# Kernel tuning notes

Measured on AMD Instinct MI355X. Metric: run time of the kernel, lower is better.

Reference implementation:

```python
import jax, jax.numpy as jnp
import numpy as np

B, T, D, H = 4, 2048, 1024, 16
HD = D // H  # head_dim = 64

def setup_inputs() -> dict:
    key = jax.random.key(0)
    k1, k2, k3 = jax.random.split(key, 3)
    x = jax.random.normal(k1, (B, T, D), dtype=jnp.float32)
    Wqkv = jax.random.normal(k2, (D, 3 * D), dtype=jnp.float32) * (D ** -0.5)
    Wout = jax.random.normal(k3, (D, D), dtype=jnp.float32) * (D ** -0.5)
    return {"x": x, "Wqkv": Wqkv, "Wout": Wout}

def reference(x, Wqkv, Wout):
    Bb, Tt, C = x.shape
    qkv = x @ Wqkv  # [B,T,3D]
    qkv = qkv.reshape(Bb, Tt, 3, H, HD)
    q, k, v = qkv[:, :, 0], qkv[:, :, 1], qkv[:, :, 2]  # each [B,T,H,HD]
    scale = 1.0 / np.sqrt(HD)
    # scores [B,H,T,T]
    attn = jnp.einsum('bqhd,bkhd->bhqk', q, k) * scale
    causal = jnp.tril(jnp.ones((Tt, Tt), dtype=bool))
    attn = jnp.where(causal[None, None], attn, -jnp.inf)
    attn = jax.nn.softmax(attn, axis=-1)
    out = jnp.einsum('bhqk,bkhd->bqhd', attn, v).reshape(Bb, Tt, C)
    return out @ Wout
```

## Files before the change

### kernel.cpp

```cpp
#include <hip/hip_runtime.h>
#include <hip/hip_bf16.h>

#define T_SEQ 2048
#define NBATCH 4
#define NHEAD 16
#define HDIM 64
#define DMODEL 1024

typedef __bf16 bf16x8 __attribute__((ext_vector_type(8)));
typedef float f32x4 __attribute__((ext_vector_type(4)));
typedef float f32x16 __attribute__((ext_vector_type(16)));

__device__ __forceinline__ unsigned short f2bf(float f) {
  unsigned int u = __builtin_bit_cast(unsigned int, f);
  u += 0x7fffu + ((u >> 16) & 1u);
  return (unsigned short)(u >> 16);
}

__device__ __forceinline__ float fexp2(float x) {
  float r;
  asm("v_exp_f32 %0, %1" : "=v"(r) : "v"(x));
  return r;
}

__device__ __forceinline__ void async_cp16(void* lds, const void* g) {
  __builtin_amdgcn_global_load_lds((const __attribute__((address_space(1))) void*)g,
                                   (__attribute__((address_space(3))) void*)lds,
                                   16, 0, 0);
}

__global__ __launch_bounds__(256) void conv_bf16_k(const float* __restrict__ in,
                                                   unsigned short* __restrict__ out, int n) {
  int i = (blockIdx.x * 256 + threadIdx.x) * 4;
  if (i >= n) return;
  float4 v = *(const float4*)(in + i);
  ushort4 o;
  o.x = f2bf(v.x); o.y = f2bf(v.y); o.z = f2bf(v.z); o.w = f2bf(v.w);
  *(ushort4*)(out + i) = o;
}

__global__ __launch_bounds__(256) void transpose_bf16_k(const float* __restrict__ in,
                                                        unsigned short* __restrict__ out,
                                                        int R, int C) {
  __shared__ float tile[32][33];
  int c0 = blockIdx.x * 32, r0 = blockIdx.y * 32;
  int tx = threadIdx.x, ty = threadIdx.y;
#pragma unroll
  for (int j = 0; j < 32; j += 8)
    tile[ty + j][tx] = in[(size_t)(r0 + ty + j) * C + c0 + tx];
  __syncthreads();
#pragma unroll
  for (int j = 0; j < 32; j += 8)
    out[(size_t)(c0 + ty + j) * R + r0 + tx] = f2bf(tile[tx][ty + j]);
}

template <int EPI, int NT>
__global__ __launch_bounds__(512, 1) void gemm_8ph2_k(const unsigned short* __restrict__ A,
                                                      const unsigned short* __restrict__ Bt,
                                                      unsigned short* __restrict__ Qb,
                                                      unsigned short* __restrict__ Kb,
                                                      unsigned short* __restrict__ Vt,
                                                      float* __restrict__ Cout) {
  __shared__ uint4 ldsv[6144];
  char* lds = (char*)ldsv;
  const int t = threadIdx.x;
  const int w = t >> 6, lane = t & 63;
  const int lr = lane & 15, lg = lane >> 4;
  const int wr = w >> 1, wc = w & 1;
  const int bid = blockIdx.x;
  const int perx = (NT * 32) / 8;
  const int wid = (bid & 7) * perx + (bid >> 3);
  const int m0 = (wid / NT) * 256, n0 = (wid % NT) * 128;

  const int row0 = t >> 3;
  const int colc0 = (t & 7) ^ (row0 & 7);
  const int stU = w * 1024;

  const unsigned short* Abase = A + (size_t)(m0 + row0) * 1024 + colc0 * 8;
  const unsigned short* Bbase = Bt + (size_t)(n0 + row0) * 1024 + colc0 * 8;

#define STGA(dst, h, kt)                                                        \
  {                                                                             \
    const unsigned short* _s = Abase + (size_t)(h) * 128 * 1024 + (kt) * 64;    \
    async_cp16(lds + (dst) + (h) * 16384 + stU, _s);                            \
    async_cp16(lds + (dst) + (h) * 16384 + stU + 8192, _s + 64 * 1024);         \
  }
#define STGB(dst, kt)                                                           \
  {                                                                             \
    const unsigned short* _s = Bbase + (kt) * 64;                               \
    async_cp16(lds + (dst) + 32768 + stU, _s);                                  \
    async_cp16(lds + (dst) + 32768 + stU + 8192, _s + 64 * 1024);               \
  }
#define VM2() asm volatile("s_waitcnt vmcnt(2)" ::: "memory")
#define BAR()                                                                   \
  {                                                                             \
    __builtin_amdgcn_s_barrier();                                               \
    __builtin_amdgcn_sched_barrier(0);                                          \
  }

  f32x4 acc[4][4];
#pragma unroll
  for (int mi = 0; mi < 4; ++mi)
#pragma unroll
    for (int ni = 0; ni < 4; ++ni) acc[mi][ni] = (f32x4){0.f, 0.f, 0.f, 0.f};

  STGA(0, 0, 0);
  STGA(0, 1, 0);
  STGB(0, 0);
  STGB(49152, 1);
  VM2();
  BAR();

  bf16x8 bfr[4][2], af[2][2];
  const int ldsAh = (wr >> 1) * 16384;
  const int arow0 = (wr & 1) * 64;
  const int brow0 = wc * 64;

#define LDB(pbase)                                                                   \
  {                                                                                  \
    _Pragma("unroll") for (int ni = 0; ni < 4; ++ni) _Pragma("unroll")               \
        for (int kk = 0; kk < 2; ++kk) {                                             \
      int rrow = brow0 + ni * 16 + lr;                                               \
      int cc = (kk * 4 + lg) ^ (lr & 7);                                             \
      bfr[ni][kk] = *(const bf16x8*)(lds + (pbase) + 32768 + rrow * 128 + cc * 16);  \
    }                                                                                \
  }
#define LDA(Q, pbase)                                                                \
  {                                                                                  \
    _Pragma("unroll") for (int m2 = 0; m2 < 2; ++m2) _Pragma("unroll")               \
        for (int kk = 0; kk < 2; ++kk) {                                             \
      int rrow = arow0 + (2 * (Q) + m2) * 16 + lr;                                   \
      int cc = (kk * 4 + lg) ^ (lr & 7);                                             \
      af[m2][kk] = *(const bf16x8*)(lds + (pbase) + ldsAh + rrow * 128 + cc * 16);   \
    }                                                                                \
  }
#define MM(Q)                                                                        \
  {                                                                                  \
    __builtin_amdgcn_s_setprio(1);                                                   \
    _Pragma("unroll") for (int m2 = 0; m2 < 2; ++m2) _Pragma("unroll")               \
        for (int kk = 0; kk < 2; ++kk) _Pragma("unroll") for (int ni = 0; ni < 4;    \
                                                              ++ni) acc[2 * (Q) +    \
                                                                        m2][ni] =    \
            __builtin_amdgcn_mfma_f32_16x16x32_bf16(af[m2][kk], bfr[ni][kk],         \
                                                    acc[2 * (Q) + m2][ni], 0, 0, 0); \
    __builtin_amdgcn_s_setprio(0);                                                   \
  }

  for (int I = 0; I < 8; ++I) {
    const int t1o = 2 * I + 1;
    const int t2e = (2 * I + 2 < 16) ? 2 * I + 2 : 15;
    const int t3o = (2 * I + 3 < 16) ? 2 * I + 3 : 15;
    LDB(0); LDA(0, 0); STGA(49152, 0, t1o); BAR(); MM(0); BAR();
    LDA(1, 0); STGA(49152, 1, t1o); STGB(0, t2e); BAR(); MM(1); VM2(); BAR();
    LDB(49152); LDA(0, 49152); STGA(0, 0, t2e); BAR(); MM(0); BAR();
    LDA(1, 49152); STGA(0, 1, t2e); STGB(49152, t3o); BAR(); MM(1); VM2(); BAR();
  }

#pragma unroll
  for (int mi = 0; mi < 4; ++mi) {
#pragma unroll
    for (int ni = 0; ni < 4; ++ni) {
      int gm = m0 + wr * 64 + mi * 16 + lg * 4;
      int gn = n0 + wc * 64 + ni * 16 + lr;
      f32x4 v = acc[mi][ni];
      if (EPI == 0) {
        int b = gm >> 11, tt = gm & 2047;
        int sel = gn >> 10, rem = gn & 1023;
        int h = rem >> 6, hd = rem & 63;
        int bh = b * NHEAD + h;
        if (sel == 0) {
          unsigned short* p = Qb + ((size_t)bh * T_SEQ + tt) * HDIM + hd;
#pragma unroll
          for (int r = 0; r < 4; ++r)
            p[(size_t)r * HDIM] = f2bf(v[r] * (0.125f * 1.44269504f));
        } else if (sel == 1) {
          unsigned short* p = Kb + (size_t)bh * T_SEQ * HDIM + (tt >> 5) * 2048 +
                              (hd >> 4) * 512 + ((hd >> 3) & 1) * 256 + (tt & 31) * 8 +
                              (hd & 7);
#pragma unroll
          for (int r = 0; r < 4; ++r) p[r * 8] = f2bf(v[r]);
        } else {
          unsigned short* p = Vt + (size_t)bh * T_SEQ * HDIM + (tt >> 4) * 1024 +
                              ((tt >> 3) & 1) * 512 + (hd >> 5) * 256 + (hd & 31) * 8 +
                              (tt & 7);
          ushort4 o;
          o.x = f2bf(v[0]); o.y = f2bf(v[1]); o.z = f2bf(v[2]); o.w = f2bf(v[3]);
          *(ushort4*)p = o;
        }
      } else {
#pragma unroll
        for (int r = 0; r < 4; ++r) Cout[(size_t)(gm + r) * (NT * 128) + gn] = v[r];
      }
    }
  }
#undef STGA
#undef STGB
#undef VM2
#undef BAR
#undef LDB
#undef LDA
#undef MM
}

#define PVJJ(Sv, B, JJ, Oa, Obb)                                                              \
  {                                                                                           \
    unsigned w0, w1, w2, w3;                                                                  \
    asm("v_cvt_pk_bf16_f32 %0, %1, %2" : "=v"(w0) : "v"(Sv[B + 0]), "v"(Sv[B + 1]));          \
    asm("v_cvt_pk_bf16_f32 %0, %1, %2" : "=v"(w1) : "v"(Sv[B + 2]), "v"(Sv[B + 3]));          \
    asm("v_cvt_pk_bf16_f32 %0, %1, %2" : "=v"(w2) : "v"(Sv[B + 4]), "v"(Sv[B + 5]));          \
    asm("v_cvt_pk_bf16_f32 %0, %1, %2" : "=v"(w3) : "v"(Sv[B + 6]), "v"(Sv[B + 7]));          \
    asm("v_permlane32_swap_b32 %0, %1" : "+v"(w0), "+v"(w2));                                 \
    asm("v_permlane32_swap_b32 %0, %1" : "+v"(w1), "+v"(w3));                                 \
    union { unsigned u[4]; bf16x8 v; } pf;                                                    \
    pf.u[0] = w0; pf.u[1] = w1; pf.u[2] = w2; pf.u[3] = w3;                                   \
    bf16x8 vfa = *(const bf16x8*)(bv + (JJ) * 2048 + hi * 1024 + lq * 16);                    \
    bf16x8 vfb = *(const bf16x8*)(bv + (JJ) * 2048 + hi * 1024 + lq * 16 + 512);              \
    __builtin_amdgcn_s_setprio(1);                                                            \
    Oa = __builtin_amdgcn_mfma_f32_32x32x16_bf16(vfa, pf.v, Oa, 0, 0, 0);                     \
    Obb = __builtin_amdgcn_mfma_f32_32x32x16_bf16(vfb, pf.v, Obb, 0, 0, 0);                   \
    __builtin_amdgcn_s_setprio(0);                                                            \
  }

__global__ __launch_bounds__(512, 2) void attn_fwd9_k(const unsigned short* __restrict__ Qb,
                                                      const unsigned short* __restrict__ Kb,
                                                      const unsigned short* __restrict__ Vt,
                                                      unsigned short* __restrict__ Ob) {
  __shared__ char lds[32768];
  const int tid = threadIdx.x;
  const int w = tid >> 6, lane = tid & 63;
  const int lq = lane & 31, hi = lane >> 5;
  const int bid = blockIdx.x;
  const int xcd = bid & 7, i = bid >> 3;
  const int bh = xcd * 8 + (i & 7);
  const int s = (i < 32) ? 7 - (i >> 3) : (i >> 3) - 4;
  const int qb = s * 8 + w;
  const int qw = qb * 32;
  const int P = 4 * (s + 1);

  const unsigned short* Qp = Qb + (size_t)bh * T_SEQ * HDIM;
  const char* Ksrc = (const char*)(Kb + (size_t)bh * T_SEQ * HDIM);
  const char* Vsrc = (const char*)(Vt + (size_t)bh * T_SEQ * HDIM);
  const int b = bh >> 4, h = bh & 15;

#define ASTG(bb, p)                                                                  \
  {                                                                                  \
    async_cp16(lds + (bb) * 16384 + w * 1024, Ksrc + (size_t)(p) * 8192 + tid * 16); \
    async_cp16(lds + (bb) * 16384 + 8192 + w * 1024,                                 \
               Vsrc + (size_t)(p) * 8192 + tid * 16);                                \
  }

  bf16x8 qf[4];
#pragma unroll
  for (int dj = 0; dj < 4; ++dj)
    qf[dj] = *(const bf16x8*)(Qp + (size_t)(qw + lq) * HDIM + dj * 16 + hi * 8);

  f32x16 O0, O1;
#pragma unroll
  for (int r = 0; r < 16; ++r) { O0[r] = 0.f; O1[r] = 0.f; }
  float m_run = -30000.0f, l_run = 0.f;

  auto smax_pair = [&](f32x16& S0, f32x16& S1) {
    float m8[8];
#pragma unroll
    for (int r = 0; r < 8; ++r)
      m8[r] = fmaxf(fmaxf(S0[r], S0[r + 8]), fmaxf(S1[r], S1[r + 8]));
#pragma unroll
    for (int r = 0; r < 4; ++r) m8[r] = fmaxf(m8[r], m8[r + 4]);
    float pmax = fmaxf(fmaxf(m8[0], m8[1]), fmaxf(m8[2], m8[3]));
    pmax = fmaxf(pmax, __shfl_xor(pmax, 32, 64));
    if (__any(pmax > m_run + 11.5f)) {
      float mn = fmaxf(m_run, pmax);
      float al = fexp2(m_run - mn);
      m_run = mn;
      l_run *= al;
#pragma unroll
      for (int r = 0; r < 16; ++r) { O0[r] *= al; O1[r] *= al; }
    }
#pragma unroll
    for (int r = 0; r < 16; ++r) {
      S0[r] = fexp2(S0[r] - m_run);
      S1[r] = fexp2(S1[r] - m_run);
    }
    float s8[8];
#pragma unroll
    for (int r = 0; r < 8; ++r) s8[r] = (S0[r] + S0[r + 8]) + (S1[r] + S1[r + 8]);
#pragma unroll
    for (int r = 0; r < 4; ++r) s8[r] += s8[r + 4];
    float ps = (s8[0] + s8[1]) + (s8[2] + s8[3]);
    ps += __shfl_xor(ps, 32, 64);
    l_run += ps;
  };

  auto smax_single = [&](f32x16& S0) {
    float m8[8];
#pragma unroll
    for (int r = 0; r < 8; ++r) m8[r] = fmaxf(S0[r], S0[r + 8]);
#pragma unroll
    for (int r = 0; r < 4; ++r) m8[r] = fmaxf(m8[r], m8[r + 4]);
    float pmax = fmaxf(fmaxf(m8[0], m8[1]), fmaxf(m8[2], m8[3]));
    pmax = fmaxf(pmax, __shfl_xor(pmax, 32, 64));
    if (__any(pmax > m_run + 11.5f)) {
      float mn = fmaxf(m_run, pmax);
      float al = fexp2(m_run - mn);
      m_run = mn;
      l_run *= al;
#pragma unroll
      for (int r = 0; r < 16; ++r) { O0[r] *= al; O1[r] *= al; }
    }
#pragma unroll
    for (int r = 0; r < 16; ++r) S0[r] = fexp2(S0[r] - m_run);
    float s8[8];
#pragma unroll
    for (int r = 0; r < 8; ++r) s8[r] = S0[r] + S0[r + 8];
#pragma unroll
    for (int r = 0; r < 4; ++r) s8[r] += s8[r + 4];
    float ps = (s8[0] + s8[1]) + (s8[2] + s8[3]);
    ps += __shfl_xor(ps, 32, 64);
    l_run += ps;
  };

  ASTG(0, 0);
  __syncthreads();

  for (int p = 0; p < P; ++p) {
    if (p + 1 < P) ASTG((p + 1) & 1, p + 1);
    const char* bk = lds + (p & 1) * 16384;
    const char* bv = bk + 8192;
    const int t0 = 2 * p, t1 = 2 * p + 1;
    if (t0 <= qb) {
      const bool v1 = (t1 <= qb);
      f32x16 S0, S1;
#pragma unroll
      for (int r = 0; r < 16; ++r) { S0[r] = 0.f; S1[r] = 0.f; }
      __builtin_amdgcn_s_setprio(1);
#pragma unroll
      for (int dj = 0; dj < 4; ++dj) {
        bf16x8 k0 = *(const bf16x8*)(bk + dj * 1024 + lane * 16);
        S0 = __builtin_amdgcn_mfma_f32_32x32x16_bf16(k0, qf[dj], S0, 0, 0, 0);
      }
      if (v1) {
#pragma unroll
        for (int dj = 0; dj < 4; ++dj) {
          bf16x8 k1 = *(const bf16x8*)(bk + 4096 + dj * 1024 + lane * 16);
          S1 = __builtin_amdgcn_mfma_f32_32x32x16_bf16(k1, qf[dj], S1, 0, 0, 0);
        }
      }
      __builtin_amdgcn_s_setprio(0);
      if (t0 == qb) {
#pragma unroll
        for (int r = 0; r < 16; ++r) {
          int kvl = (r & 3) + 8 * (r >> 2) + 4 * hi;
          S0[r] = (kvl > lq) ? -30000.0f : S0[r];
        }
      }
      if (v1 && t1 == qb) {
#pragma unroll
        for (int r = 0; r < 16; ++r) {
          int kvl = (r & 3) + 8 * (r >> 2) + 4 * hi;
          S1[r] = (kvl > lq) ? -30000.0f : S1[r];
        }
      }
      if (v1) {
        smax_pair(S0, S1);
        PVJJ(S0, 0, 0, O0, O1); PVJJ(S0, 8, 1, O0, O1);
        PVJJ(S1, 0, 2, O0, O1); PVJJ(S1, 8, 3, O0, O1);
      } else {
        smax_single(S0);
        PVJJ(S0, 0, 0, O0, O1); PVJJ(S0, 8, 1, O0, O1);
      }
    }
    __syncthreads();
  }

  const float linv = 1.0f / l_run;
  unsigned short* op = Ob + ((size_t)(b * T_SEQ + qw + lq)) * DMODEL + h * HDIM;
#pragma unroll
  for (int g = 0; g < 4; ++g) {
    ushort4 o;
    o.x = f2bf(O0[4 * g + 0] * linv);
    o.y = f2bf(O0[4 * g + 1] * linv);
    o.z = f2bf(O0[4 * g + 2] * linv);
    o.w = f2bf(O0[4 * g + 3] * linv);
    *(ushort4*)(op + 8 * g + 4 * hi) = o;
    ushort4 o2;
    o2.x = f2bf(O1[4 * g + 0] * linv);
    o2.y = f2bf(O1[4 * g + 1] * linv);
    o2.z = f2bf(O1[4 * g + 2] * linv);
    o2.w = f2bf(O1[4 * g + 3] * linv);
    *(ushort4*)(op + 32 + 8 * g + 4 * hi) = o2;
  }
#undef ASTG
}

extern "C" void kernel_launch(void* const* d_in, const int* in_sizes, int n_in,
                              void* d_out, int out_size, void* d_ws, size_t ws_size,
                              hipStream_t stream) {
  const float* x = (const float*)d_in[0];
  const float* Wqkv = (const float*)d_in[1];
  const float* Wout = (const float*)d_in[2];
  float* out = (float*)d_out;

  unsigned short* ws = (unsigned short*)d_ws;
  const size_t nx = (size_t)NBATCH * T_SEQ * DMODEL;
  unsigned short* xb    = ws;
  unsigned short* wqkvT = xb + nx;
  unsigned short* woutT = wqkvT + (size_t)3 * DMODEL * DMODEL;
  unsigned short* Qb    = woutT + (size_t)DMODEL * DMODEL;
  unsigned short* Kb    = Qb + nx;
  unsigned short* Vt    = Kb + nx;
  unsigned short* Ab    = Vt + nx;
  size_t need = 2ull * (5 * nx + 4ull * DMODEL * DMODEL);
  if (ws_size < need) return;

  conv_bf16_k<<<dim3((unsigned)(nx / 1024)), dim3(256), 0, stream>>>(x, xb, (int)nx);
  transpose_bf16_k<<<dim3(3 * DMODEL / 32, DMODEL / 32), dim3(32, 8), 0, stream>>>(
      Wqkv, wqkvT, DMODEL, 3 * DMODEL);
  transpose_bf16_k<<<dim3(DMODEL / 32, DMODEL / 32), dim3(32, 8), 0, stream>>>(
      Wout, woutT, DMODEL, DMODEL);
  gemm_8ph2_k<0, 24><<<dim3(768), dim3(512), 0, stream>>>(xb, wqkvT, Qb, Kb, Vt, nullptr);
  attn_fwd9_k<<<dim3(512), dim3(512), 0, stream>>>(Qb, Kb, Vt, Ab);
  gemm_8ph2_k<1, 8><<<dim3(256), dim3(512), 0, stream>>>(Ab, woutT, nullptr, nullptr,
                                                         nullptr, out);
}
```

Before: 155.9 us.

## Use dedicated 256x192-tile QKV projection GEMM with new pipelined staging

Replaces the templated QKV GEMM (768 blocks of 256x128 tiles) with a dedicated kernel using 256x192 tiles over 512 blocks. Each wave computes a 64x96 sub-tile, and A and B staging is interleaved across four MFMA phases per buffer half. The aim is better operand reuse per LDS load and fewer blocks, which should fit the 256-CU grid more evenly, at the cost of more accumulator registers and more LDS. The old GEMM keeps only the output-projection epilogue.

```diff
diff --git a/kernel.cpp b/kernel.cpp
--- a/kernel.cpp
+++ b/kernel.cpp
@@ -52,6 +52,142 @@
 #pragma unroll
   for (int j = 0; j < 32; j += 8)
     out[(size_t)(c0 + ty + j) * R + r0 + tx] = f2bf(tile[tx][ty + j]);
+}
+
+__global__ __launch_bounds__(512, 1) void gemm1_v3_k(const unsigned short* __restrict__ A,
+                                                     const unsigned short* __restrict__ Bt,
+                                                     unsigned short* __restrict__ Qb,
+                                                     unsigned short* __restrict__ Kb,
+                                                     unsigned short* __restrict__ Vt) {
+  __shared__ uint4 ldsv[7168];
+  char* lds = (char*)ldsv;
+  const int t = threadIdx.x;
+  const int w = t >> 6, lane = t & 63;
+  const int lr = lane & 15, lg = lane >> 4;
+  const int wr = w >> 1, wc = w & 1;
+  const int bid = blockIdx.x;
+  const int wid = (bid & 7) * 64 + (bid >> 3);
+  const int m0 = (wid >> 4) * 256, n0 = (wid & 15) * 192;
+
+  const int row0 = t >> 3;
+  const int colc0 = (t & 7) ^ (row0 & 7);
+  const int stU = w * 1024;
+
+  const unsigned short* Abase = A + (size_t)(m0 + row0) * 1024 + colc0 * 8;
+  const unsigned short* Bbase = Bt + (size_t)(n0 + row0) * 1024 + colc0 * 8;
+
+#define STGA(pb, h, kt)                                                          \
+  async_cp16(lds + (pb) + (h) * 8192 + stU,                                      \
+             Abase + (size_t)(h) * 64 * 1024 + (kt) * 64)
+#define STGB(pb, s, kt)                                                          \
+  async_cp16(lds + (pb) + 32768 + (s) * 8192 + stU,                              \
+             Bbase + (size_t)(s) * 64 * 1024 + (kt) * 64)
+#define VM3() asm volatile("s_waitcnt vmcnt(3)" ::: "memory")
+#define BAR()                                                                    \
+  {                                                                              \
+    __builtin_amdgcn_s_barrier();                                                \
+    __builtin_amdgcn_sched_barrier(0);                                           \
+  }
+
+  f32x4 acc[4][6];
+#pragma unroll
+  for (int mi = 0; mi < 4; ++mi)
+#pragma unroll
+    for (int ni = 0; ni < 6; ++ni) acc[mi][ni] = (f32x4){0.f, 0.f, 0.f, 0.f};
+
+  STGA(0, 0, 0); STGA(0, 1, 0); STGA(0, 2, 0); STGA(0, 3, 0);
+  STGB(0, 0, 0); STGB(0, 1, 0); STGB(0, 2, 0);
+  STGB(57344, 0, 1); STGB(57344, 1, 1); STGB(57344, 2, 1);
+  VM3();
+  BAR();
+
+  bf16x8 bfr[6][2], af[2];
+
+#define LDB(pb)                                                                      \
+  {                                                                                  \
+    _Pragma("unroll") for (int ni = 0; ni < 6; ++ni) _Pragma("unroll")               \
+        for (int kk = 0; kk < 2; ++kk) {                                             \
+      int rrow = wc * 96 + ni * 16 + lr;                                             \
+      int cc = (kk * 4 + lg) ^ (lr & 7);                                             \
+      bfr[ni][kk] = *(const bf16x8*)(lds + (pb) + 32768 + rrow * 128 + cc * 16);     \
+    }                                                                                \
+  }
+#define LDA(Q, pb)                                                                   \
+  {                                                                                  \
+    _Pragma("unroll") for (int kk = 0; kk < 2; ++kk) {                               \
+      int rrow = wr * 64 + (Q) * 16 + lr;                                            \
+      int cc = (kk * 4 + lg) ^ (lr & 7);                                             \
+      af[kk] = *(const bf16x8*)(lds + (pb) + rrow * 128 + cc * 16);                  \
+    }                                                                                \
+  }
+#define MM(Q)                                                                        \
+  {                                                                                  \
+    __builtin_amdgcn_s_setprio(1);                                                   \
+    _Pragma("unroll") for (int kk = 0; kk < 2; ++kk) _Pragma("unroll")               \
+        for (int ni = 0; ni < 6; ++ni) acc[Q][ni] =                                  \
+            __builtin_amdgcn_mfma_f32_16x16x32_bf16(af[kk], bfr[ni][kk],             \
+                                                    acc[Q][ni], 0, 0, 0);            \
+    __builtin_amdgcn_s_setprio(0);                                                   \
+  }
+
+  const int P0 = 0, P1 = 57344;
+  for (int I = 0; I < 8; ++I) {
+    const int t1 = 2 * I + 1;
+    const int t2 = (2 * I + 2 < 16) ? 2 * I + 2 : 15;
+    const int t3 = (2 * I + 3 < 16) ? 2 * I + 3 : 15;
+    LDB(P0); LDA(0, P0); STGA(P1, 0, t1); STGA(P1, 1, t1); BAR(); MM(0); BAR();
+    LDA(1, P0); STGA(P1, 2, t1); STGA(P1, 3, t1); BAR(); MM(1); BAR();
+    LDA(2, P0); STGB(P0, 0, t2); STGB(P0, 1, t2); BAR(); MM(2); BAR();
+    LDA(3, P0); STGB(P0, 2, t2); BAR(); MM(3);
+    VM3();
+    BAR();
+    LDB(P1); LDA(0, P1); STGA(P0, 0, t2); STGA(P0, 1, t2); BAR(); MM(0); BAR();
+    LDA(1, P1); STGA(P0, 2, t2); STGA(P0, 3, t2); BAR(); MM(1); BAR();
+    LDA(2, P1); STGB(P1, 0, t3); STGB(P1, 1, t3); BAR(); MM(2); BAR();
+    LDA(3, P1); STGB(P1, 2, t3); BAR(); MM(3);
+    VM3();
+    BAR();
+  }
+
+#pragma unroll
+  for (int mi = 0; mi < 4; ++mi) {
+#pragma unroll
+    for (int ni = 0; ni < 6; ++ni) {
+      int gm = m0 + wr * 64 + mi * 16 + lg * 4;
+      int gn = n0 + wc * 96 + ni * 16 + lr;
+      f32x4 v = acc[mi][ni];
+      int b = gm >> 11, tt = gm & 2047;
+      int sel = gn >> 10, rem = gn & 1023;
+      int h = rem >> 6, hd = rem & 63;
+      int bh = b * NHEAD + h;
+      if (sel == 0) {
+        unsigned short* p = Qb + ((size_t)bh * T_SEQ + tt) * HDIM + hd;
+#pragma unroll
+        for (int r = 0; r < 4; ++r)
+          p[(size_t)r * HDIM] = f2bf(v[r] * (0.125f * 1.44269504f));
+      } else if (sel == 1) {
+        unsigned short* p = Kb + (size_t)bh * T_SEQ * HDIM + (tt >> 5) * 2048 +
+                            (hd >> 4) * 512 + ((hd >> 3) & 1) * 256 + (tt & 31) * 8 +
+                            (hd & 7);
+#pragma unroll
+        for (int r = 0; r < 4; ++r) p[r * 8] = f2bf(v[r]);
+      } else {
+        unsigned short* p = Vt + (size_t)bh * T_SEQ * HDIM + (tt >> 4) * 1024 +
+                            ((tt >> 3) & 1) * 512 + (hd >> 5) * 256 + (hd & 31) * 8 +
+                            (tt & 7);
+        ushort4 o;
+        o.x = f2bf(v[0]); o.y = f2bf(v[1]); o.z = f2bf(v[2]); o.w = f2bf(v[3]);
+        *(ushort4*)p = o;
+      }
+    }
+  }
+#undef STGA
+#undef STGB
+#undef VM3
+#undef BAR
+#undef LDB
+#undef LDA
+#undef MM
 }
 
 template <int EPI, int NT>
@@ -163,34 +299,8 @@
       int gm = m0 + wr * 64 + mi * 16 + lg * 4;
       int gn = n0 + wc * 64 + ni * 16 + lr;
       f32x4 v = acc[mi][ni];
-      if (EPI == 0) {
-        int b = gm >> 11, tt = gm & 2047;
-        int sel = gn >> 10, rem = gn & 1023;
-        int h = rem >> 6, hd = rem & 63;
-        int bh = b * NHEAD + h;
-        if (sel == 0) {
-          unsigned short* p = Qb + ((size_t)bh * T_SEQ + tt) * HDIM + hd;
-#pragma unroll
-          for (int r = 0; r < 4; ++r)
-            p[(size_t)r * HDIM] = f2bf(v[r] * (0.125f * 1.44269504f));
-        } else if (sel == 1) {
-          unsigned short* p = Kb + (size_t)bh * T_SEQ * HDIM + (tt >> 5) * 2048 +
-                              (hd >> 4) * 512 + ((hd >> 3) & 1) * 256 + (tt & 31) * 8 +
-                              (hd & 7);
-#pragma unroll
-          for (int r = 0; r < 4; ++r) p[r * 8] = f2bf(v[r]);
-        } else {
-          unsigned short* p = Vt + (size_t)bh * T_SEQ * HDIM + (tt >> 4) * 1024 +
-                              ((tt >> 3) & 1) * 512 + (hd >> 5) * 256 + (hd & 31) * 8 +
-                              (tt & 7);
-          ushort4 o;
-          o.x = f2bf(v[0]); o.y = f2bf(v[1]); o.z = f2bf(v[2]); o.w = f2bf(v[3]);
-          *(ushort4*)p = o;
-        }
-      } else {
-#pragma unroll
-        for (int r = 0; r < 4; ++r) Cout[(size_t)(gm + r) * (NT * 128) + gn] = v[r];
-      }
+#pragma unroll
+      for (int r = 0; r < 4; ++r) Cout[(size_t)(gm + r) * (NT * 128) + gn] = v[r];
     }
   }
 #undef STGA
@@ -417,7 +527,7 @@
       Wqkv, wqkvT, DMODEL, 3 * DMODEL);
   transpose_bf16_k<<<dim3(DMODEL / 32, DMODEL / 32), dim3(32, 8), 0, stream>>>(
       Wout, woutT, DMODEL, DMODEL);
-  gemm_8ph2_k<0, 24><<<dim3(768), dim3(512), 0, stream>>>(xb, wqkvT, Qb, Kb, Vt, nullptr);
+  gemm1_v3_k<<<dim3(512), dim3(512), 0, stream>>>(xb, wqkvT, Qb, Kb, Vt);
   attn_fwd9_k<<<dim3(512), dim3(512), 0, stream>>>(Qb, Kb, Vt, Ab);
   gemm_8ph2_k<1, 8><<<dim3(256), dim3(512), 0, stream>>>(Ab, woutT, nullptr, nullptr,
                                                          nullptr, out);
```

After: 146.5 us. -6.0%, faster.
